# Kernel optimization log

Hardware: AMD Instinct MI355X
Metric: run time of the kernel (lower is better)

The kernel has to match this reference:

```python
import jax, jax.numpy as jnp
import numpy as np

N_NODES = 100000
N_EDGES = 1600000
IN_DIM = 256
OUT_DIM = 128
EPS = 1e-12  # torch F.normalize default eps


def setup_inputs() -> dict:
    key = jax.random.key(0)
    k1, k2, k3, k4, k5 = jax.random.split(key, 5)
    x = jax.random.normal(k1, (N_NODES, IN_DIM), dtype=jnp.float32)
    edge_index = jax.random.randint(k2, (2, N_EDGES), 0, N_NODES, dtype=jnp.int64)
    # projection (no bias): weight [out, in]
    Wp = jax.random.normal(k3, (OUT_DIM, IN_DIM), dtype=jnp.float32) * 0.05
    # GCNConv internal linear weight [out, out] and output bias [out]
    Wg = jax.random.normal(k4, (OUT_DIM, OUT_DIM), dtype=jnp.float32) * 0.05
    bg = jax.random.normal(k5, (OUT_DIM,), dtype=jnp.float32) * 0.01
    return {"x": x, "edge_index": edge_index, "Wp": Wp, "Wg": Wg, "bg": bg}


def reference(x, edge_index, Wp, Wg, bg):
    n = x.shape[0]
    # projection: x @ Wp^T
    h = x @ Wp.T                      # [N, OUT]
    # GCNConv: transform first, then propagate
    h = h @ Wg.T                      # [N, OUT]
    # add self-loops
    loops = jnp.arange(n, dtype=edge_index.dtype)
    row = jnp.concatenate([edge_index[0], loops])   # source
    col = jnp.concatenate([edge_index[1], loops])   # target
    # symmetric normalization: deg over target index (edge_weight = 1)
    deg = jax.ops.segment_sum(jnp.ones_like(col, dtype=h.dtype), col, num_segments=n)
    dinv = jnp.where(deg > 0, jax.lax.rsqrt(deg), 0.0)
    norm = dinv[row] * dinv[col]                     # [E+N]
    # gather messages from source, scale, scatter-add to target
    msg = h[row] * norm[:, None]                     # [E+N, OUT]
    out = jax.ops.segment_sum(msg, col, num_segments=n)  # [N, OUT]
    out = out + bg
    # F.normalize(dim=1): divide by L2 norm clamped at eps
    nrm = jnp.sqrt(jnp.sum(out * out, axis=1, keepdims=True))
    out = out / jnp.maximum(nrm, EPS)
    return out
```

## Files before the change

### kernel.cpp

```cpp
#include <hip/hip_runtime.h>
#include <hip/hip_fp16.h>

#define NDIM 128
#define KDIM 256
#define MT 5
#define AROW 264
#define CHUNK 6400
#define MAXBUCK 128

typedef _Float16 half8 __attribute__((ext_vector_type(8)));
typedef float float4v __attribute__((ext_vector_type(4)));

__global__ void k_combine_w(const float* __restrict__ Wp, const float* __restrict__ Wg,
                            _Float16* __restrict__ Bfrag) {
    int o = blockIdx.x;
    int i = threadIdx.x;
    float acc = 0.f;
#pragma unroll 4
    for (int k = 0; k < 128; ++k) acc = fmaf(Wg[o * 128 + k], Wp[k * 256 + i], acc);
    int kk = i >> 5, r = i & 31, quad = r >> 3, j = r & 7;
    int ntile = o >> 4, lanen = o & 15, lane = quad * 16 + lanen;
    Bfrag[(((ntile * 8 + kk) * 64) + lane) * 8 + j] = (_Float16)acc;
}

__global__ __launch_bounds__(256) void k_phase1(const int* __restrict__ col, int E,
                                                int* __restrict__ hist, int NBLK, int NBUCK) {
    __shared__ int h[MAXBUCK];
    int tid = threadIdx.x;
    if (tid < MAXBUCK) h[tid] = 0;
    __syncthreads();
    int e0 = blockIdx.x * CHUNK;
    int e1 = min(e0 + CHUNK, E);
    for (int e = e0 + tid; e < e1; e += 256) atomicAdd(&h[col[e] >> 10], 1);
    __syncthreads();
    if (tid < NBUCK) hist[tid * NBLK + blockIdx.x] = h[tid];
}

__global__ __launch_bounds__(1024) void k_scan2(int* __restrict__ hist, int NE) {
    __shared__ int s[1024];
    int t = threadIdx.x;
    int CH = (NE + 1023) >> 10;
    int off = t * CH;
    int sum = 0;
    for (int j = 0; j < CH; ++j) { int idx = off + j; if (idx < NE) sum += hist[idx]; }
    s[t] = sum;
    __syncthreads();
    for (int d = 1; d < 1024; d <<= 1) {
        int y = (t >= d) ? s[t - d] : 0;
        __syncthreads();
        s[t] += y;
        __syncthreads();
    }
    int run = s[t] - sum;
    for (int j = 0; j < CH; ++j) {
        int idx = off + j;
        if (idx < NE) { int v = hist[idx]; hist[idx] = run; run += v; }
    }
}

__global__ __launch_bounds__(256) void k_phase3(const int* __restrict__ ei, int E,
                                                const int* __restrict__ offs, int NBLK, int NBUCK,
                                                int2* __restrict__ tmp) {
    __shared__ int cur[MAXBUCK];
    int tid = threadIdx.x;
    if (tid < NBUCK) cur[tid] = offs[tid * NBLK + blockIdx.x];
    __syncthreads();
    int e0 = blockIdx.x * CHUNK;
    int e1 = min(e0 + CHUNK, E);
    for (int e = e0 + tid; e < e1; e += 256) {
        int r = ei[e];
        int c = ei[E + e];
        int p = atomicAdd(&cur[c >> 10], 1);
        tmp[p] = make_int2(r, c);
    }
}

__global__ __launch_bounds__(1024) void k_fine(const int2* __restrict__ tmp,
                                               const int* __restrict__ offs, int NBLK, int NBUCK,
                                               int N, int E,
                                               int* __restrict__ sortedRow,
                                               int* __restrict__ cnt,
                                               int* __restrict__ rowStart) {
    __shared__ int scnt[1024];
    __shared__ int cur[1024];
    int b = blockIdx.x;
    int t = threadIdx.x;
    int nodeBase = b << 10;
    int start = offs[b * NBLK];
    int end = (b + 1 < NBUCK) ? offs[(b + 1) * NBLK] : E;

    scnt[t] = 0;
    __syncthreads();
    for (int p = start + t; p < end; p += 1024) atomicAdd(&scnt[tmp[p].y - nodeBase], 1);
    __syncthreads();
    int v = scnt[t];
    for (int d = 1; d < 1024; d <<= 1) {
        int y = (t >= d) ? scnt[t - d] : 0;
        __syncthreads();
        scnt[t] += y;
        __syncthreads();
    }
    int excl = scnt[t] - v;
    int node = nodeBase + t;
    if (node < N) {
        cnt[node] = v;
        rowStart[node] = start + excl;
    }
    cur[t] = start + excl;
    __syncthreads();
    for (int p = start + t; p < end; p += 1024) {
        int2 pr = tmp[p];
        int slot = atomicAdd(&cur[pr.y - nodeBase], 1);
        sortedRow[slot] = pr.x;
    }
    if (b == NBUCK - 1 && t == 0) rowStart[N] = E;
}

__global__ __launch_bounds__(256) void k_gemm_mfma(const float* __restrict__ x,
                                                   const _Float16* __restrict__ Bfrag,
                                                   const int* __restrict__ cnt,
                                                   _Float16* __restrict__ g, int nrows) {
    __shared__ __align__(16) _Float16 xs[16 * AROW];
    int tid  = threadIdx.x;
    int lane = tid & 63;
    int w    = tid >> 6;
    int quad = lane >> 4;
    int lcol = lane & 15;

    const half8* Bv = (const half8*)Bfrag;
    half8 b0[8], b1[8];
#pragma unroll
    for (int kk = 0; kk < 8; ++kk) {
        b0[kk] = Bv[(w * 8 + kk) * 64 + lane];
        b1[kk] = Bv[((w + 4) * 8 + kk) * 64 + lane];
    }

    long base = (long)blockIdx.x * (16 * MT);
    for (int t = 0; t < MT; ++t) {
        long m0 = base + t * 16;
        __syncthreads();
        const float4* xv = (const float4*)(x + m0 * KDIM);
#pragma unroll
        for (int ii = 0; ii < 4; ++ii) {
            int idx = tid + ii * 256;
            int m = idx >> 6, k4 = idx & 63;
            float4 v = xv[idx];
            _Float16* d = &xs[m * AROW + k4 * 4];
            d[0] = (_Float16)v.x; d[1] = (_Float16)v.y;
            d[2] = (_Float16)v.z; d[3] = (_Float16)v.w;
        }
        __syncthreads();

        float4v acc0 = {0.f, 0.f, 0.f, 0.f}, acc1 = {0.f, 0.f, 0.f, 0.f};
#pragma unroll
        for (int kk = 0; kk < 8; ++kk) {
            half8 a = *(const half8*)(&xs[lcol * AROW + kk * 32 + quad * 8]);
            acc0 = __builtin_amdgcn_mfma_f32_16x16x32_f16(a, b0[kk], acc0, 0, 0, 0);
            acc1 = __builtin_amdgcn_mfma_f32_16x16x32_f16(a, b1[kk], acc1, 0, 0, 0);
        }

#pragma unroll
        for (int r = 0; r < 4; ++r) {
            long node = m0 + quad * 4 + r;
            float di = rsqrtf((float)(cnt[node] + 1));
            g[node * NDIM + w * 16 + lcol]        = (_Float16)(acc0[r] * di);
            g[node * NDIM + (w + 4) * 16 + lcol]  = (_Float16)(acc1[r] * di);
        }
    }
}

__global__ __launch_bounds__(256) void k_gather(const __half2* __restrict__ g,
                                                const int* __restrict__ rowStart,
                                                const int* __restrict__ sortedRow,
                                                const int* __restrict__ cnt,
                                                const float* __restrict__ bg,
                                                float* __restrict__ out) {
    int lane = threadIdx.x & 63;
    int i = blockIdx.x * 4 + (threadIdx.x >> 6);
    const int s = rowStart[i];
    const int e = rowStart[i + 1];
    const size_t stride = NDIM / 2;

    __half2 self = g[(size_t)i * stride + lane];
    float ax = __low2float(self), ay = __high2float(self);

    int p = s;
    for (; p + 4 <= e; p += 4) {
        int r0 = sortedRow[p + 0];
        int r1 = sortedRow[p + 1];
        int r2 = sortedRow[p + 2];
        int r3 = sortedRow[p + 3];
        __half2 m0 = g[(size_t)r0 * stride + lane];
        __half2 m1 = g[(size_t)r1 * stride + lane];
        __half2 m2 = g[(size_t)r2 * stride + lane];
        __half2 m3 = g[(size_t)r3 * stride + lane];
        ax += __low2float(m0) + __low2float(m1) + __low2float(m2) + __low2float(m3);
        ay += __high2float(m0) + __high2float(m1) + __high2float(m2) + __high2float(m3);
    }
    for (; p < e; ++p) {
        int r = sortedRow[p];
        __half2 m = g[(size_t)r * stride + lane];
        ax += __low2float(m);
        ay += __high2float(m);
    }

    float di = rsqrtf((float)(cnt[i] + 1));
    float2 b = ((const float2*)bg)[lane];
    float v0 = fmaf(di, ax, b.x);
    float v1 = fmaf(di, ay, b.y);

    float sq = v0 * v0 + v1 * v1;
#pragma unroll
    for (int d = 32; d > 0; d >>= 1) sq += __shfl_xor(sq, d);
    float scale = 1.0f / fmaxf(sqrtf(sq), 1e-12f);
    ((float2*)out)[(size_t)i * stride + lane] = make_float2(v0 * scale, v1 * scale);
}

extern "C" void kernel_launch(void* const* d_in, const int* in_sizes, int n_in,
                              void* d_out, int out_size, void* d_ws, size_t ws_size,
                              hipStream_t stream) {
    const float* x  = (const float*)d_in[0];
    const int*   ei = (const int*)  d_in[1];
    const float* Wp = (const float*)d_in[2];
    const float* Wg = (const float*)d_in[3];
    const float* bg = (const float*)d_in[4];
    float* out = (float*)d_out;

    const int N = in_sizes[0] / KDIM;
    const int E = in_sizes[1] / 2;

    const int NBLK  = (E + CHUNK - 1) / CHUNK;
    const int NBUCK = (N + 1023) >> 10;
    const int NE    = NBLK * NBUCK;

    char* p = (char*)d_ws;
    auto carve = [&](size_t bytes) { void* r = (void*)p; p += (bytes + 255) & ~(size_t)255; return r; };
    _Float16* g      = (_Float16*)carve((size_t)N * NDIM * 2);
    int*   sortedRow = (int*)  carve((size_t)E * 4);
    int2*  tmp       = (int2*) carve((size_t)E * 8);
    _Float16* Bfrag  = (_Float16*)carve((size_t)KDIM * NDIM * 2);
    int*   cnt       = (int*)  carve((size_t)N * 4);
    int*   rowStart  = (int*)  carve((size_t)(N + 1) * 4);
    int*   hist      = (int*)  carve((size_t)NE * 4);

    hipLaunchKernelGGL(k_combine_w, dim3(NDIM), dim3(KDIM), 0, stream, Wp, Wg, Bfrag);
    hipLaunchKernelGGL(k_phase1, dim3(NBLK), dim3(256), 0, stream, ei + E, E, hist, NBLK, NBUCK);
    hipLaunchKernelGGL(k_scan2, dim3(1), dim3(1024), 0, stream, hist, NE);
    hipLaunchKernelGGL(k_phase3, dim3(NBLK), dim3(256), 0, stream, ei, E, hist, NBLK, NBUCK, tmp);
    hipLaunchKernelGGL(k_fine, dim3(NBUCK), dim3(1024), 0, stream, tmp, hist, NBLK, NBUCK, N, E,
                       sortedRow, cnt, rowStart);
    hipLaunchKernelGGL(k_gemm_mfma, dim3(N / (16 * MT)), dim3(256), 0, stream, x, Bfrag, cnt, g, N);
    hipLaunchKernelGGL(k_gather, dim3(N / 4), dim3(256), 0, stream,
                       (const __half2*)g, rowStart, sortedRow, cnt, bg, out);
}
```

Measured before the change: 363.5 us.

## Gather four neighbor rows per wavefront with 16-byte loads in k_gather

Restructures the gather so each wavefront splits into four 16-lane groups. Each group loads one full 256-byte fp16 neighbor row as half8 vectors, so four edges are processed at once instead of one row per 64 lanes of 4-byte loads. Partial sums are combined across the groups with cross-lane shuffles, then the self term, bias and L2 normalization are applied and one group writes the row with float4 stores. This is meant to raise memory-level parallelism and cut load instruction count, in exchange for more registers and extra shuffle reductions.

```diff
diff --git a/kernel.cpp b/kernel.cpp
--- a/kernel.cpp
+++ b/kernel.cpp
@@ -169,7 +169,7 @@
     }
 }
 
-__global__ __launch_bounds__(256) void k_gather(const __half2* __restrict__ g,
+__global__ __launch_bounds__(256) void k_gather(const _Float16* __restrict__ g,
                                                 const int* __restrict__ rowStart,
                                                 const int* __restrict__ sortedRow,
                                                 const int* __restrict__ cnt,
@@ -179,41 +179,80 @@
     int i = blockIdx.x * 4 + (threadIdx.x >> 6);
     const int s = rowStart[i];
     const int e = rowStart[i + 1];
-    const size_t stride = NDIM / 2;
-
-    __half2 self = g[(size_t)i * stride + lane];
-    float ax = __low2float(self), ay = __high2float(self);
+    const int g4  = lane >> 4;
+    const int r16 = lane & 15;
+
+    const half8* __restrict__ gv = (const half8*)g;
+
+    float acc[8];
+#pragma unroll
+    for (int j = 0; j < 8; ++j) acc[j] = 0.f;
 
     int p = s;
+    for (; p + 16 <= e; p += 16) {
+        int r0 = sortedRow[p + g4];
+        int r1 = sortedRow[p + 4 + g4];
+        int r2 = sortedRow[p + 8 + g4];
+        int r3 = sortedRow[p + 12 + g4];
+        half8 v0 = gv[(size_t)r0 * 16 + r16];
+        half8 v1 = gv[(size_t)r1 * 16 + r16];
+        half8 v2 = gv[(size_t)r2 * 16 + r16];
+        half8 v3 = gv[(size_t)r3 * 16 + r16];
+#pragma unroll
+        for (int j = 0; j < 8; ++j)
+            acc[j] += ((float)v0[j] + (float)v1[j]) + ((float)v2[j] + (float)v3[j]);
+    }
     for (; p + 4 <= e; p += 4) {
-        int r0 = sortedRow[p + 0];
-        int r1 = sortedRow[p + 1];
-        int r2 = sortedRow[p + 2];
-        int r3 = sortedRow[p + 3];
-        __half2 m0 = g[(size_t)r0 * stride + lane];
-        __half2 m1 = g[(size_t)r1 * stride + lane];
-        __half2 m2 = g[(size_t)r2 * stride + lane];
-        __half2 m3 = g[(size_t)r3 * stride + lane];
-        ax += __low2float(m0) + __low2float(m1) + __low2float(m2) + __low2float(m3);
-        ay += __high2float(m0) + __high2float(m1) + __high2float(m2) + __high2float(m3);
-    }
-    for (; p < e; ++p) {
-        int r = sortedRow[p];
-        __half2 m = g[(size_t)r * stride + lane];
-        ax += __low2float(m);
-        ay += __high2float(m);
-    }
+        int r0 = sortedRow[p + g4];
+        half8 v0 = gv[(size_t)r0 * 16 + r16];
+#pragma unroll
+        for (int j = 0; j < 8; ++j) acc[j] += (float)v0[j];
+    }
+    if (p + g4 < e) {
+        int r0 = sortedRow[p + g4];
+        half8 v0 = gv[(size_t)r0 * 16 + r16];
+#pragma unroll
+        for (int j = 0; j < 8; ++j) acc[j] += (float)v0[j];
+    }
+
+#pragma unroll
+    for (int j = 0; j < 8; ++j) {
+        acc[j] += __shfl_xor(acc[j], 16);
+        acc[j] += __shfl_xor(acc[j], 32);
+    }
+
+    half8 sv = gv[(size_t)i * 16 + r16];
+#pragma unroll
+    for (int j = 0; j < 8; ++j) acc[j] += (float)sv[j];
 
     float di = rsqrtf((float)(cnt[i] + 1));
-    float2 b = ((const float2*)bg)[lane];
-    float v0 = fmaf(di, ax, b.x);
-    float v1 = fmaf(di, ay, b.y);
-
-    float sq = v0 * v0 + v1 * v1;
-#pragma unroll
-    for (int d = 32; d > 0; d >>= 1) sq += __shfl_xor(sq, d);
+    float4 b0 = ((const float4*)bg)[r16 * 2];
+    float4 b1 = ((const float4*)bg)[r16 * 2 + 1];
+    float v[8];
+    v[0] = fmaf(di, acc[0], b0.x);
+    v[1] = fmaf(di, acc[1], b0.y);
+    v[2] = fmaf(di, acc[2], b0.z);
+    v[3] = fmaf(di, acc[3], b0.w);
+    v[4] = fmaf(di, acc[4], b1.x);
+    v[5] = fmaf(di, acc[5], b1.y);
+    v[6] = fmaf(di, acc[6], b1.z);
+    v[7] = fmaf(di, acc[7], b1.w);
+
+    float sq = 0.f;
+#pragma unroll
+    for (int j = 0; j < 8; ++j) sq += v[j] * v[j];
+    sq += __shfl_xor(sq, 1);
+    sq += __shfl_xor(sq, 2);
+    sq += __shfl_xor(sq, 4);
+    sq += __shfl_xor(sq, 8);
     float scale = 1.0f / fmaxf(sqrtf(sq), 1e-12f);
-    ((float2*)out)[(size_t)i * stride + lane] = make_float2(v0 * scale, v1 * scale);
+
+    if (g4 == 0) {
+        float4 o0 = make_float4(v[0] * scale, v[1] * scale, v[2] * scale, v[3] * scale);
+        float4 o1 = make_float4(v[4] * scale, v[5] * scale, v[6] * scale, v[7] * scale);
+        ((float4*)out)[(size_t)i * 32 + r16 * 2]     = o0;
+        ((float4*)out)[(size_t)i * 32 + r16 * 2 + 1] = o1;
+    }
 }
 
 extern "C" void kernel_launch(void* const* d_in, const int* in_sizes, int n_in,
@@ -251,5 +290,5 @@
                        sortedRow, cnt, rowStart);
     hipLaunchKernelGGL(k_gemm_mfma, dim3(N / (16 * MT)), dim3(256), 0, stream, x, Bfrag, cnt, g, N);
     hipLaunchKernelGGL(k_gather, dim3(N / 4), dim3(256), 0, stream,
-                       (const __half2*)g, rowStart, sortedRow, cnt, bg, out);
-}
+                       g, rowStart, sortedRow, cnt, bg, out);
+}
```

Result: faster. 353.5 us (-2.8%).
